# Optimization experiments

Measured on AMD Instinct MI355X. Metric: run time of the kernel, lower is better.

The kernel has to match this reference:

```python
import jax, jax.numpy as jnp
import numpy as np

N, K = 50000, 16          # nodes, fixed neighbor-list length
IN, HID, OUT = 11, 64, 1  # temporal feat dim, hidden, output


def setup_inputs() -> dict:
    key = jax.random.key(0)
    ks = iter(jax.random.split(key, 64))
    def rn(shape, scale=1.0):
        return jax.random.normal(next(ks), shape, dtype=jnp.float32) * scale
    inp = {
        "x": rn((N, IN)),
        "neighbors": jax.random.randint(next(ks), (N, K), 0, N, dtype=jnp.int32),
        "prev_hidden": rn((N, HID)),
    }
    # DGL SAGEConv(lstm): LSTM(in=d, hid=d), fc_self Linear(d,o,bias=True), fc_neigh Linear(d,o,bias=False)
    dims = [(IN, HID), (HID, HID), (HID, HID), (HID, OUT)]
    for li, (d, o) in enumerate(dims, start=1):
        s = 1.0 / np.sqrt(d)
        inp[f"l{li}_Wih"] = rn((4 * d, d), s)
        inp[f"l{li}_Whh"] = rn((4 * d, d), s)
        inp[f"l{li}_bih"] = rn((4 * d,), s)
        inp[f"l{li}_bhh"] = rn((4 * d,), s)
        inp[f"l{li}_Ws"] = rn((o, d), s)
        inp[f"l{li}_bs"] = rn((o,), s)
        inp[f"l{li}_Wn"] = rn((o, d), s)
    sg = 1.0 / np.sqrt(HID)
    inp["g_Wih"] = rn((3 * HID, HID), sg)
    inp["g_Whh"] = rn((3 * HID, HID), sg)
    inp["g_bih"] = rn((3 * HID,), sg)
    inp["g_bhh"] = rn((3 * HID,), sg)
    return inp


def _sage_conv(h, neighbors, Wih, Whh, bih, bhh, Ws, bs, Wn):
    """DGL SAGEConv with aggregator_type='lstm'."""
    m = h[neighbors]             # [N, K, D] gathered neighbor messages
    ms = jnp.swapaxes(m, 0, 1)   # [K, N, D] time-major for scan
    Nn, D = h.shape
    h0 = jnp.zeros((Nn, D), h.dtype)

    def step(carry, mt):
        hp, cp = carry
        g = mt @ Wih.T + bih + hp @ Whh.T + bhh   # [N, 4D]
        i, f, gg, o = jnp.split(g, 4, axis=-1)    # torch LSTM gate order i,f,g,o
        c = jax.nn.sigmoid(f) * cp + jax.nn.sigmoid(i) * jnp.tanh(gg)
        hn = jax.nn.sigmoid(o) * jnp.tanh(c)
        return (hn, c), None

    (hK, _), _ = jax.lax.scan(step, (h0, h0), ms)  # final hidden state = neighbor agg
    return h @ Ws.T + bs + hK @ Wn.T


def _gru(x, h, Wih, Whh, bih, bhh):
    """torch.nn.GRUCell, gate order r,z,n."""
    gi = x @ Wih.T + bih
    gh = h @ Whh.T + bhh
    ir, iz, inn = jnp.split(gi, 3, axis=-1)
    hr, hz, hn = jnp.split(gh, 3, axis=-1)
    r = jax.nn.sigmoid(ir + hr)
    z = jax.nn.sigmoid(iz + hz)
    n = jnp.tanh(inn + r * hn)
    return (1.0 - z) * n + z * h


def reference(x, neighbors, prev_hidden,
              l1_Wih, l1_Whh, l1_bih, l1_bhh, l1_Ws, l1_bs, l1_Wn,
              l2_Wih, l2_Whh, l2_bih, l2_bhh, l2_Ws, l2_bs, l2_Wn,
              l3_Wih, l3_Whh, l3_bih, l3_bhh, l3_Ws, l3_bs, l3_Wn,
              l4_Wih, l4_Whh, l4_bih, l4_bhh, l4_Ws, l4_bs, l4_Wn,
              g_Wih, g_Whh, g_bih, g_bhh):
    h = jax.nn.relu(_sage_conv(x, neighbors, l1_Wih, l1_Whh, l1_bih, l1_bhh, l1_Ws, l1_bs, l1_Wn))
    h = jax.nn.relu(_sage_conv(h, neighbors, l2_Wih, l2_Whh, l2_bih, l2_bhh, l2_Ws, l2_bs, l2_Wn))
    h = jax.nn.relu(_sage_conv(h, neighbors, l3_Wih, l3_Whh, l3_bih, l3_bhh, l3_Ws, l3_bs, l3_Wn))
    h = _gru(h, prev_hidden, g_Wih, g_Whh, g_bih, g_bhh)
    logits = _sage_conv(h, neighbors, l4_Wih, l4_Whh, l4_bih, l4_bhh, l4_Ws, l4_bs, l4_Wn)
    return logits
```

## Files before the change

### kernel.cpp

```cpp
#include <hip/hip_runtime.h>

#define N_NODES 50000

typedef __bf16 bf16x8 __attribute__((ext_vector_type(8)));
typedef float f32x4 __attribute__((ext_vector_type(4)));

union U16x8 { uint4 v; unsigned short u[8]; bf16x8 b; };

__device__ __forceinline__ float b2f(unsigned short h){
  unsigned int u = ((unsigned int)h) << 16;
  return __builtin_bit_cast(float, u);
}
__device__ __forceinline__ unsigned short f2b(float x){
  unsigned int u = __builtin_bit_cast(unsigned int, x);
  u = u + 0x7FFFu + ((u >> 16) & 1u);
  return (unsigned short)(u >> 16);
}
__device__ __forceinline__ float sigm(float x){
  const float e = __builtin_amdgcn_exp2f(x * -1.4426950408889634f);
  return __builtin_amdgcn_rcpf(1.0f + e);
}
__device__ __forceinline__ float tanh_(float x){
  const float e = __builtin_amdgcn_exp2f(x * 2.8853900817779268f);
  return fmaf(-2.0f, __builtin_amdgcn_rcpf(1.0f + e), 1.0f);
}

__device__ __forceinline__ bf16x8 load8_bf16(const float* p){
  float4 a = *(const float4*)p; float4 c = *(const float4*)(p + 4);
  U16x8 r;
  r.u[0]=f2b(a.x); r.u[1]=f2b(a.y); r.u[2]=f2b(a.z); r.u[3]=f2b(a.w);
  r.u[4]=f2b(c.x); r.u[5]=f2b(c.y); r.u[6]=f2b(c.z); r.u[7]=f2b(c.w);
  return r.b;
}


__global__ __launch_bounds__(256) void l1_kernel(
    const float* __restrict__ x, const int* __restrict__ nbr,
    const float* __restrict__ Wih, const float* __restrict__ Whh,
    const float* __restrict__ bih, const float* __restrict__ bhh,
    const float* __restrict__ Ws,  const float* __restrict__ bs,
    const float* __restrict__ Wn,  unsigned short* __restrict__ out_hl)
{
  __shared__ unsigned short mbuf[16][2][16][24];
  __shared__ unsigned short hbuf[2][2][16][24];

  const int tid  = threadIdx.x;
  const int wave = tid >> 6, lane = tid & 63;
  const int n16  = lane & 15, q = lane >> 4;
  const int nb0  = blockIdx.x * 16;

  { unsigned int* p = (unsigned int*)hbuf;
    for (int i = tid; i < 768; i += 256) p[i] = 0u; }

  {
    const int nd = tid >> 4, t = tid & 15;
    const int gn = nbr[(nb0 + nd) * 16 + t];
    const float* row = x + (long)gn * 11;
    float v[16];
    #pragma unroll
    for (int j = 0; j < 11; j++) v[j] = row[j];
    #pragma unroll
    for (int j = 11; j < 16; j++) v[j] = 0.f;
    #pragma unroll
    for (int j = 0; j < 16; j++){
      unsigned short hb = f2b(v[j]);
      mbuf[t][0][nd][j] = hb;
      mbuf[t][1][nd][j] = f2b(v[j] - b2f(hb));
    }
  }

  bf16x8 wf[4];
  float bg4[4];
  #pragma unroll
  for (int g = 0; g < 4; g++){
    const int u = n16;
    const float* src = (q < 2) ? (Wih + (g * 11 + u) * 11)
                               : (Whh + (g * 11 + u) * 11);
    const int kb = (q & 1) * 8;
    U16x8 a;
    #pragma unroll
    for (int j = 0; j < 8; j++){
      const int k = kb + j;
      float v = (u < 11 && k < 11) ? src[k] : 0.f;
      a.u[j] = f2b(v);
    }
    wf[g] = a.b;
    bg4[g] = (n16 < 11) ? (bih[g * 11 + n16] + bhh[g * 11 + n16]) : 0.f;
  }

  float c_ = 0.f;
  __syncthreads();

  for (int t = 0; t < 16; t++){
    const int db = t & 1, nb = db ^ 1;

    const unsigned short* ph = (q < 2) ? &mbuf[t][0][n16][q * 8]
                                       : &hbuf[db][0][n16][(q - 2) * 8];
    U16x8 ah, al;
    ah.v = *(const uint4*)ph;
    al.v = *(const uint4*)(ph + 384);

    f32x4 acc[4];
    #pragma unroll
    for (int g = 0; g < 4; g++){
      f32x4 av = {bg4[g], bg4[g], bg4[g], bg4[g]};
      acc[g] = __builtin_amdgcn_mfma_f32_16x16x32_bf16(ah.b, wf[g], av, 0, 0, 0);
      acc[g] = __builtin_amdgcn_mfma_f32_16x16x32_bf16(al.b, wf[g], acc[g], 0, 0, 0);
    }

    {
      const int r = wave;
      const float iv = sigm(acc[0][r]);
      const float fv = sigm(acc[1][r]);
      const float gg = tanh_(acc[2][r]);
      const float ov = sigm(acc[3][r]);
      c_ = fv * c_ + iv * gg;
      const float hv = ov * tanh_(c_);
      const unsigned short hb = f2b(hv);
      hbuf[nb][0][q * 4 + wave][n16] = hb;
      hbuf[nb][1][q * 4 + wave][n16] = f2b(hv - b2f(hb));
    }
    __syncthreads();
  }

  U16x8 eah, eal;
  if (q < 2){
    const float* row = x + (long)(nb0 + n16) * 11;
    U16x8 H, L;
    #pragma unroll
    for (int j = 0; j < 8; j++){
      const int k = q * 8 + j;
      float v = (k < 11) ? row[k] : 0.f;
      unsigned short hb = f2b(v); H.u[j] = hb; L.u[j] = f2b(v - b2f(hb));
    }
    eah = H; eal = L;
  } else {
    const unsigned short* ph = &hbuf[0][0][n16][(q - 2) * 8];
    eah.v = *(const uint4*)ph;
    eal.v = *(const uint4*)(ph + 384);
  }

  bf16x8 ewf;
  {
    const int uo = wave * 16 + n16;
    const float* src = (q < 2) ? (Ws + uo * 11) : (Wn + uo * 11);
    const int kb = (q & 1) * 8;
    U16x8 a;
    #pragma unroll
    for (int j = 0; j < 8; j++){
      const int k = kb + j;
      a.u[j] = f2b((k < 11) ? src[k] : 0.f);
    }
    ewf = a.b;
  }

  {
    const int uo = wave * 16 + n16;
    const float bsv = bs[uo];
    f32x4 e = {bsv, bsv, bsv, bsv};
    e = __builtin_amdgcn_mfma_f32_16x16x32_bf16(eah.b, ewf, e, 0, 0, 0);
    e = __builtin_amdgcn_mfma_f32_16x16x32_bf16(eal.b, ewf, e, 0, 0, 0);
    #pragma unroll
    for (int r = 0; r < 4; r++){
      const float vv = fmaxf(e[r], 0.f);
      out_hl[(size_t)(nb0 + q * 4 + r) * 64 + uo] = f2b(vv);
    }
  }
}

__global__ __launch_bounds__(256, 3) void sage64_kernel(
    const unsigned short* __restrict__ in_hl, const int* __restrict__ nbr,
    const float* __restrict__ Wih, const float* __restrict__ Whh,
    const float* __restrict__ bih, const float* __restrict__ bhh,
    const float* __restrict__ Ws,  const float* __restrict__ bs,
    const float* __restrict__ Wn,
    unsigned short* __restrict__ out_hl, float* __restrict__ out_f32, int mode)
{
  __shared__ uint4 mbuf[16][16][8];
  __shared__ uint4 hbuf[2][16][8];

  const int tid = threadIdx.x;
  const int wv = tid >> 6, lane = tid & 63;
  const int n16 = lane & 15, q = lane >> 4;
  const int nb0 = blockIdx.x * 16;

  {
    const int nd = tid >> 4, t = tid & 15;
    const int gn = nbr[(nb0 + nd) * 16 + t];
    const uint4* src = (const uint4*)(in_hl + (size_t)gn * 64);
    #pragma unroll
    for (int s = 0; s < 8; s++)
      mbuf[t][nd][(s + nd + t) & 7] = src[s];
  }
  { unsigned int* p = (unsigned int*)&hbuf[0][0][0];
    for (int i = tid; i < 512; i += 256) p[i] = 0u; }

  bf16x8 wih_f[4][2], whh_f[4][2];
  #pragma unroll
  for (int g = 0; g < 4; g++){
    const int row = g * 64 + wv * 16 + n16;
    #pragma unroll
    for (int kc = 0; kc < 2; kc++){
      wih_f[g][kc] = load8_bf16(Wih + row * 64 + kc * 32 + q * 8);
      whh_f[g][kc] = load8_bf16(Whh + row * 64 + kc * 32 + q * 8);
    }
  }
  f32x4 bg[4];
  #pragma unroll
  for (int g = 0; g < 4; g++){
    float4 bi = *(const float4*)(bih + g * 64 + wv * 16 + q * 4);
    float4 bh = *(const float4*)(bhh + g * 64 + wv * 16 + q * 4);
    f32x4 s = {bi.x + bh.x, bi.y + bh.y, bi.z + bh.z, bi.w + bh.w};
    bg[g] = s;
  }

  float c4[4] = {0.f, 0.f, 0.f, 0.f};
  __syncthreads();

  for (int t = 0; t < 16; t++){
    const int db = t & 1, nbf = db ^ 1;

    bf16x8 mh[2], hh[2];
    #pragma unroll
    for (int kc = 0; kc < 2; kc++){
      U16x8 a; a.v = mbuf[t][n16][(kc * 4 + q + n16 + t) & 7]; mh[kc] = a.b;
      U16x8 c_; c_.v = hbuf[db][n16][(kc * 4 + q + n16) & 7];  hh[kc] = c_.b;
    }

    f32x4 acc[4];
    #pragma unroll
    for (int g = 0; g < 4; g++) acc[g] = bg[g];
    #pragma unroll
    for (int kc = 0; kc < 2; kc++){
      #pragma unroll
      for (int g = 0; g < 4; g++)
        acc[g] = __builtin_amdgcn_mfma_f32_16x16x32_bf16(wih_f[g][kc], mh[kc], acc[g], 0, 0, 0);
      #pragma unroll
      for (int g = 0; g < 4; g++)
        acc[g] = __builtin_amdgcn_mfma_f32_16x16x32_bf16(whh_f[g][kc], hh[kc], acc[g], 0, 0, 0);
    }

    unsigned short hB[4];
    #pragma unroll
    for (int r = 0; r < 4; r++){
      const float iv = sigm(acc[0][r]);
      const float fv = sigm(acc[1][r]);
      const float gg = tanh_(acc[2][r]);
      const float ov = sigm(acc[3][r]);
      c4[r] = fv * c4[r] + iv * gg;
      hB[r] = f2b(ov * tanh_(c4[r]));
    }
    {
      const int idx = wv * 4 + q;
      const int slot = idx >> 1, half = idx & 1;
      ((uint2*)&hbuf[nbf][n16][(slot + n16) & 7])[half] =
          make_uint2((unsigned)hB[0] | ((unsigned)hB[1] << 16),
                     (unsigned)hB[2] | ((unsigned)hB[3] << 16));
    }
    __syncthreads();
  }

  bf16x8 sH[2], kH[2];
  #pragma unroll
  for (int kc = 0; kc < 2; kc++){
    U16x8 a; a.v = *(const uint4*)(in_hl + (size_t)(nb0 + n16) * 64 + kc * 32 + q * 8);
    sH[kc] = a.b;
    U16x8 c_; c_.v = hbuf[0][n16][(kc * 4 + q + n16) & 7]; kH[kc] = c_.b;
  }

  if (mode == 0){
    bf16x8 ws_f[2], wn_f[2];
    #pragma unroll
    for (int kc = 0; kc < 2; kc++){
      ws_f[kc] = load8_bf16(Ws + (wv * 16 + n16) * 64 + kc * 32 + q * 8);
      wn_f[kc] = load8_bf16(Wn + (wv * 16 + n16) * 64 + kc * 32 + q * 8);
    }
    float4 bsv = *(const float4*)(bs + wv * 16 + q * 4);
    f32x4 e = {bsv.x, bsv.y, bsv.z, bsv.w};
    #pragma unroll
    for (int kc = 0; kc < 2; kc++){
      e = __builtin_amdgcn_mfma_f32_16x16x32_bf16(ws_f[kc], sH[kc], e, 0, 0, 0);
      e = __builtin_amdgcn_mfma_f32_16x16x32_bf16(wn_f[kc], kH[kc], e, 0, 0, 0);
    }
    unsigned short oB[4];
    #pragma unroll
    for (int r = 0; r < 4; r++) oB[r] = f2b(fmaxf(e[r], 0.f));
    *(uint2*)(out_hl + (size_t)(nb0 + n16) * 64 + wv * 16 + q * 4) =
        make_uint2((unsigned)oB[0] | ((unsigned)oB[1] << 16),
                   (unsigned)oB[2] | ((unsigned)oB[3] << 16));
  } else {
    if (wv == 0){
      bf16x8 ws_f[2], wn_f[2];
      #pragma unroll
      for (int kc = 0; kc < 2; kc++){
        U16x8 a, b_;
        a.v = make_uint4(0u,0u,0u,0u); b_.v = make_uint4(0u,0u,0u,0u);
        if (n16 == 0){
          a.b  = load8_bf16(Ws + kc * 32 + q * 8);
          b_.b = load8_bf16(Wn + kc * 32 + q * 8);
        }
        ws_f[kc] = a.b; wn_f[kc] = b_.b;
      }
      f32x4 e = {0.f, 0.f, 0.f, 0.f};
      #pragma unroll
      for (int kc = 0; kc < 2; kc++){
        e = __builtin_amdgcn_mfma_f32_16x16x32_bf16(ws_f[kc], sH[kc], e, 0, 0, 0);
        e = __builtin_amdgcn_mfma_f32_16x16x32_bf16(wn_f[kc], kH[kc], e, 0, 0, 0);
      }
      if (q == 0) out_f32[nb0 + n16] = e[0] + bs[0];
    }
  }
}

__global__ __launch_bounds__(256) void gru_kernel(
    const unsigned short* __restrict__ h3_hl, const float* __restrict__ prev,
    const float* __restrict__ gWih, const float* __restrict__ gWhh,
    const float* __restrict__ gbih, const float* __restrict__ gbhh,
    unsigned short* __restrict__ out_hl)
{
  const int tid = threadIdx.x, wave = tid >> 6, lane = tid & 63;
  const int n16 = lane & 15, q = lane >> 4;
  const int nb0 = blockIdx.x * 16;
  const int u_ = wave * 16 + n16;

  bf16x8 ah[2], ap[2];
  #pragma unroll
  for (int kc = 0; kc < 2; kc++){
    U16x8 a; a.v = *(const uint4*)(h3_hl + (size_t)(nb0 + n16) * 64 + kc * 32 + q * 8);
    ah[kc] = a.b;
    ap[kc] = load8_bf16(prev + (size_t)(nb0 + n16) * 64 + kc * 32 + q * 8);
  }

  bf16x8 wi_f[3][2], wh_f[3][2];
  #pragma unroll
  for (int g = 0; g < 3; g++){
    const int row = g * 64 + wave * 16 + n16;
    #pragma unroll
    for (int kc = 0; kc < 2; kc++){
      wi_f[g][kc] = load8_bf16(gWih + row * 64 + kc * 32 + q * 8);
      wh_f[g][kc] = load8_bf16(gWhh + row * 64 + kc * 32 + q * 8);
    }
  }

  f32x4 gi[3], gh[3];
  #pragma unroll
  for (int g = 0; g < 3; g++){
    const float bi = gbih[g * 64 + u_], bh = gbhh[g * 64 + u_];
    f32x4 vi = {bi, bi, bi, bi}; gi[g] = vi;
    f32x4 vh = {bh, bh, bh, bh}; gh[g] = vh;
  }
  #pragma unroll
  for (int kc = 0; kc < 2; kc++){
    #pragma unroll
    for (int g = 0; g < 3; g++)
      gi[g] = __builtin_amdgcn_mfma_f32_16x16x32_bf16(ah[kc], wi_f[g][kc], gi[g], 0, 0, 0);
    #pragma unroll
    for (int g = 0; g < 3; g++)
      gh[g] = __builtin_amdgcn_mfma_f32_16x16x32_bf16(ap[kc], wh_f[g][kc], gh[g], 0, 0, 0);
  }

  #pragma unroll
  for (int r = 0; r < 4; r++){
    const long node = nb0 + q * 4 + r;
    const float rv = sigm(gi[0][r] + gh[0][r]);
    const float zv = sigm(gi[1][r] + gh[1][r]);
    const float nv = tanh_(gi[2][r] + rv * gh[2][r]);
    const float hp = prev[node * 64 + u_];
    const float v = (1.f - zv) * nv + zv * hp;
    out_hl[(size_t)node * 64 + u_] = f2b(v);
  }
}

extern "C" void kernel_launch(void* const* d_in, const int* in_sizes, int n_in,
                              void* d_out, int out_size, void* d_ws, size_t ws_size,
                              hipStream_t stream)
{
  (void)in_sizes; (void)n_in; (void)out_size; (void)ws_size;
  const float* x    = (const float*)d_in[0];
  const int*   nbr  = (const int*)d_in[1];
  const float* prev = (const float*)d_in[2];
  auto W = [&](int i){ return (const float*)d_in[i]; };

  unsigned short* tabA = (unsigned short*)d_ws;
  unsigned short* tabB = tabA + (size_t)N_NODES * 64;

  l1_kernel<<<N_NODES / 16, 256, 0, stream>>>(
      x, nbr, W(3), W(4), W(5), W(6), W(7), W(8), W(9), tabA);
  sage64_kernel<<<N_NODES / 16, 256, 0, stream>>>(
      tabA, nbr, W(10), W(11), W(12), W(13), W(14), W(15), W(16), tabB, nullptr, 0);
  sage64_kernel<<<N_NODES / 16, 256, 0, stream>>>(
      tabB, nbr, W(17), W(18), W(19), W(20), W(21), W(22), W(23), tabA, nullptr, 0);
  gru_kernel<<<N_NODES / 16, 256, 0, stream>>>(
      tabA, prev, W(31), W(32), W(33), W(34), tabB);
  sage64_kernel<<<N_NODES / 16, 256, 0, stream>>>(
      tabB, nbr, W(24), W(25), W(26), W(27), W(28), W(29), W(30),
      nullptr, (float*)d_out, 1);
}
```

Measured before the change: 503.7 us.

## Drop split-bf16 precision in layer 1 and halve sage64 shared buffer

Layer 1 no longer splits inputs and hidden state into high and low bf16 parts, so each step issues half the MFMAs and half the LDS traffic. The sage64 kernel keeps only 8 timesteps of gathered neighbor messages in shared memory and refills the second half at step 8. This halves its LDS footprint so the launch bound can rise from 3 to 5 blocks per CU. The costs are lower layer-1 precision, one extra barrier with an exposed gather stall midway through the recurrence, and possible register pressure at the higher occupancy target.

```diff
diff --git a/kernel.cpp b/kernel.cpp
--- a/kernel.cpp
+++ b/kernel.cpp
@@ -41,8 +41,8 @@
     const float* __restrict__ Ws,  const float* __restrict__ bs,
     const float* __restrict__ Wn,  unsigned short* __restrict__ out_hl)
 {
-  __shared__ unsigned short mbuf[16][2][16][24];
-  __shared__ unsigned short hbuf[2][2][16][24];
+  __shared__ unsigned short mbuf[16][16][24];
+  __shared__ unsigned short hbuf[2][16][24];
 
   const int tid  = threadIdx.x;
   const int wave = tid >> 6, lane = tid & 63;
@@ -50,7 +50,7 @@
   const int nb0  = blockIdx.x * 16;
 
   { unsigned int* p = (unsigned int*)hbuf;
-    for (int i = tid; i < 768; i += 256) p[i] = 0u; }
+    for (int i = tid; i < 384; i += 256) p[i] = 0u; }
 
   {
     const int nd = tid >> 4, t = tid & 15;
@@ -61,12 +61,11 @@
     for (int j = 0; j < 11; j++) v[j] = row[j];
     #pragma unroll
     for (int j = 11; j < 16; j++) v[j] = 0.f;
-    #pragma unroll
-    for (int j = 0; j < 16; j++){
-      unsigned short hb = f2b(v[j]);
-      mbuf[t][0][nd][j] = hb;
-      mbuf[t][1][nd][j] = f2b(v[j] - b2f(hb));
-    }
+    U16x8 A, B;
+    #pragma unroll
+    for (int j = 0; j < 8; j++){ A.u[j] = f2b(v[j]); B.u[j] = f2b(v[8 + j]); }
+    *(uint4*)&mbuf[t][nd][0] = A.v;
+    *(uint4*)&mbuf[t][nd][8] = B.v;
   }
 
   bf16x8 wf[4];
@@ -94,50 +93,40 @@
   for (int t = 0; t < 16; t++){
     const int db = t & 1, nb = db ^ 1;
 
-    const unsigned short* ph = (q < 2) ? &mbuf[t][0][n16][q * 8]
-                                       : &hbuf[db][0][n16][(q - 2) * 8];
-    U16x8 ah, al;
-    ah.v = *(const uint4*)ph;
-    al.v = *(const uint4*)(ph + 384);
+    const unsigned short* ph = (q < 2) ? &mbuf[t][n16][q * 8]
+                                       : &hbuf[db][n16][(q - 2) * 8];
+    U16x8 ah; ah.v = *(const uint4*)ph;
 
     f32x4 acc[4];
     #pragma unroll
     for (int g = 0; g < 4; g++){
       f32x4 av = {bg4[g], bg4[g], bg4[g], bg4[g]};
       acc[g] = __builtin_amdgcn_mfma_f32_16x16x32_bf16(ah.b, wf[g], av, 0, 0, 0);
-      acc[g] = __builtin_amdgcn_mfma_f32_16x16x32_bf16(al.b, wf[g], acc[g], 0, 0, 0);
     }
 
     {
-      const int r = wave;
-      const float iv = sigm(acc[0][r]);
-      const float fv = sigm(acc[1][r]);
-      const float gg = tanh_(acc[2][r]);
-      const float ov = sigm(acc[3][r]);
+      const float iv = sigm(acc[0][wave]);
+      const float fv = sigm(acc[1][wave]);
+      const float gg = tanh_(acc[2][wave]);
+      const float ov = sigm(acc[3][wave]);
       c_ = fv * c_ + iv * gg;
-      const float hv = ov * tanh_(c_);
-      const unsigned short hb = f2b(hv);
-      hbuf[nb][0][q * 4 + wave][n16] = hb;
-      hbuf[nb][1][q * 4 + wave][n16] = f2b(hv - b2f(hb));
+      hbuf[nb][q * 4 + wave][n16] = f2b(ov * tanh_(c_));
     }
     __syncthreads();
   }
 
-  U16x8 eah, eal;
+  U16x8 ea;
   if (q < 2){
     const float* row = x + (long)(nb0 + n16) * 11;
-    U16x8 H, L;
+    U16x8 H;
     #pragma unroll
     for (int j = 0; j < 8; j++){
       const int k = q * 8 + j;
-      float v = (k < 11) ? row[k] : 0.f;
-      unsigned short hb = f2b(v); H.u[j] = hb; L.u[j] = f2b(v - b2f(hb));
-    }
-    eah = H; eal = L;
+      H.u[j] = f2b((k < 11) ? row[k] : 0.f);
+    }
+    ea = H;
   } else {
-    const unsigned short* ph = &hbuf[0][0][n16][(q - 2) * 8];
-    eah.v = *(const uint4*)ph;
-    eal.v = *(const uint4*)(ph + 384);
+    ea.v = *(const uint4*)&hbuf[0][n16][(q - 2) * 8];
   }
 
   bf16x8 ewf;
@@ -158,17 +147,14 @@
     const int uo = wave * 16 + n16;
     const float bsv = bs[uo];
     f32x4 e = {bsv, bsv, bsv, bsv};
-    e = __builtin_amdgcn_mfma_f32_16x16x32_bf16(eah.b, ewf, e, 0, 0, 0);
-    e = __builtin_amdgcn_mfma_f32_16x16x32_bf16(eal.b, ewf, e, 0, 0, 0);
-    #pragma unroll
-    for (int r = 0; r < 4; r++){
-      const float vv = fmaxf(e[r], 0.f);
-      out_hl[(size_t)(nb0 + q * 4 + r) * 64 + uo] = f2b(vv);
-    }
-  }
-}
-
-__global__ __launch_bounds__(256, 3) void sage64_kernel(
+    e = __builtin_amdgcn_mfma_f32_16x16x32_bf16(ea.b, ewf, e, 0, 0, 0);
+    #pragma unroll
+    for (int r = 0; r < 4; r++)
+      out_hl[(size_t)(nb0 + q * 4 + r) * 64 + uo] = f2b(fmaxf(e[r], 0.f));
+  }
+}
+
+__global__ __launch_bounds__(256, 5) void sage64_kernel(
     const unsigned short* __restrict__ in_hl, const int* __restrict__ nbr,
     const float* __restrict__ Wih, const float* __restrict__ Whh,
     const float* __restrict__ bih, const float* __restrict__ bhh,
@@ -176,7 +162,7 @@
     const float* __restrict__ Wn,
     unsigned short* __restrict__ out_hl, float* __restrict__ out_f32, int mode)
 {
-  __shared__ uint4 mbuf[16][16][8];
+  __shared__ uint4 mbuf[8][16][8];
   __shared__ uint4 hbuf[2][16][8];
 
   const int tid = threadIdx.x;
@@ -184,14 +170,20 @@
   const int n16 = lane & 15, q = lane >> 4;
   const int nb0 = blockIdx.x * 16;
 
-  {
-    const int nd = tid >> 4, t = tid & 15;
-    const int gn = nbr[(nb0 + nd) * 16 + t];
+  auto refill = [&](int base){
+    const int nd = tid >> 4, sub = tid & 15;
+    const int tr = sub >> 1, half = sub & 1;
+    const int t_ = base + tr;
+    const int gn = nbr[(nb0 + nd) * 16 + t_];
     const uint4* src = (const uint4*)(in_hl + (size_t)gn * 64);
     #pragma unroll
-    for (int s = 0; s < 8; s++)
-      mbuf[t][nd][(s + nd + t) & 7] = src[s];
-  }
+    for (int j = 0; j < 4; j++){
+      const int s = half * 4 + j;
+      mbuf[tr][nd][(s + nd + t_) & 7] = src[s];
+    }
+  };
+
+  refill(0);
   { unsigned int* p = (unsigned int*)&hbuf[0][0][0];
     for (int i = tid; i < 512; i += 256) p[i] = 0u; }
 
@@ -218,13 +210,17 @@
   __syncthreads();
 
   for (int t = 0; t < 16; t++){
+    if (t == 8){
+      refill(8);
+      __syncthreads();
+    }
     const int db = t & 1, nbf = db ^ 1;
 
     bf16x8 mh[2], hh[2];
     #pragma unroll
     for (int kc = 0; kc < 2; kc++){
-      U16x8 a; a.v = mbuf[t][n16][(kc * 4 + q + n16 + t) & 7]; mh[kc] = a.b;
-      U16x8 c_; c_.v = hbuf[db][n16][(kc * 4 + q + n16) & 7];  hh[kc] = c_.b;
+      U16x8 a; a.v = mbuf[t & 7][n16][(kc * 4 + q + n16 + t) & 7]; mh[kc] = a.b;
+      U16x8 c_; c_.v = hbuf[db][n16][(kc * 4 + q + n16) & 7];      hh[kc] = c_.b;
     }
 
     f32x4 acc[4];
```

Result: slower. 957.1 us (+90.0%).
